# Performance work log

Measured on AMD Instinct MI355X. Metric: run time of the kernel, lower is better.

Reference implementation:

```python
import jax, jax.numpy as jnp
import numpy as np
from jax import lax

K2 = 3                 # support_kernel_size
TARGET_OCC = 0.5
OCC_W = 10.0
ITERS = 10             # flood-fill iterations
THRESH = 0.5
STEEP = 20.0

# 6-neighbor 3D cross kernel (plus-shaped), shape [O=1, I=1, 3, 3, 3]
_cross_np = np.zeros((1, 1, 3, 3, 3), dtype=np.float32)
for dz, dy, dx in [(0, 1, 1), (2, 1, 1), (1, 0, 1), (1, 2, 1), (1, 1, 0), (1, 1, 2)]:
    _cross_np[0, 0, dz, dy, dx] = 1.0


def _conv3d(x, k, pad):
    # x: [B, C, D, H, W], k: [O, I, kd, kh, kw]
    return lax.conv_general_dilated(
        x, k, window_strides=(1, 1, 1), padding=pad,
        dimension_numbers=('NCDHW', 'OIDHW', 'NCDHW'))


def setup_inputs() -> dict:
    key = jax.random.key(0)
    voxel_grid = jax.random.uniform(key, (4, 1, 128, 128, 128), dtype=jnp.float32)
    return {"voxel_grid": voxel_grid}


def reference(voxel_grid):
    B, C, D, H, W = voxel_grid.shape
    N = B * D * H * W
    dt = voxel_grid.dtype

    # ---- overhang score: vectorized over all z-slices at once ----
    # per-slice conv2d(3x3 ones) == conv3d with kernel depth 1
    k2 = jnp.ones((1, 1, 1, K2, K2), dt)
    below = voxel_grid[:, :, :-1]          # [B,1,D-1,H,W]
    curr = voxel_grid[:, :, 1:]
    below_support = _conv3d(below, k2, ((0, 0), (1, 1), (1, 1)))
    support_ratio = below_support / (K2 * K2)
    overhang = (curr * (1.0 - support_ratio)).sum() / N

    # ---- surface area score ----
    k3 = jnp.ones((1, 1, 3, 3, 3), dt)
    neighbor_solid = _conv3d(voxel_grid, k3, ((1, 1), (1, 1), (1, 1)))
    surface_term = neighbor_solid.sum() / 27.0 / N

    occupancy = voxel_grid.sum() / N
    occupancy_penalty = OCC_W * (occupancy - TARGET_OCC) ** 2

    # differentiable flood-fill (diff_find_enclosed_voids)
    seed = jnp.zeros_like(voxel_grid).at[:, :, 5, 5, 5].set(1.0)
    cross = jnp.asarray(_cross_np, dt)
    not_solid = 1.0 - voxel_grid

    def body(i, mask):
        c = _conv3d(mask, cross, ((1, 1), (1, 1), (1, 1)))
        act = jax.nn.sigmoid(STEEP * (c - THRESH))
        return jnp.maximum(mask, act) * not_solid

    enclosed = lax.fori_loop(0, ITERS, body, seed)
    resin_trap_penalty = 100.0 * enclosed.sum() / N

    surface_score = surface_term - resin_trap_penalty - occupancy_penalty
    return overhang, surface_score
```

## Files before the change

### kernel.cpp

```cpp
#include <hip/hip_runtime.h>

#define HW    (128*128)
#define DHW   (128*128*128)
#define NTOT  (4*DHW)
#define NBLK  1024

__device__ __forceinline__ float sigf(float x){ return 1.0f/(1.0f+__expf(-x)); }
__device__ __forceinline__ float4 ld4(const float* p){ return *(const float4*)p; }


__global__ __launch_bounds__(256, 4) void mega_k(
    const float* __restrict__ v, float* __restrict__ p_occ,
    float* __restrict__ p_surf, float* __restrict__ p_over,
    float* __restrict__ p_trap)
{
    __shared__ float4 smem4[1445];
    __shared__ float sred[16];
    float* smem = (float*)smem4;

    const int bid = blockIdx.x;
    const int tid = threadIdx.x;
    const float4 zero4 = make_float4(0,0,0,0);

    if (bid < 4) {
        const int b = bid;
        const size_t gb = (size_t)b * DHW;
        const int ty = tid & 15, tz = tid >> 4;
        const float a_lo = sigf(-10.0f), a_hi = sigf(10.0f);
        #define M(zz,yy) (smem + (((zz)*17 + (yy))*20))

        float m[16], nv[16];
        {
            const float* rv = v + gb + ((size_t)tz*128 + ty)*128;
            int dzy = abs(tz-5) + abs(ty-5);
            #pragma unroll
            for (int q = 0; q < 4; ++q) {
                int x4 = 4*q;
                float4 a = ld4(rv + x4);
                nv[x4+0]=1.f-a.x; nv[x4+1]=1.f-a.y; nv[x4+2]=1.f-a.z; nv[x4+3]=1.f-a.w;
                int d0=dzy+abs(x4+0-5), d1=dzy+abs(x4+1-5);
                int d2=dzy+abs(x4+2-5), d3=dzy+abs(x4+3-5);
                m[x4+0] = ((d0==0)?1.f:((d0==1)?a_hi:a_lo)) * nv[x4+0];
                m[x4+1] = ((d1==0)?1.f:((d1==1)?a_hi:a_lo)) * nv[x4+1];
                m[x4+2] = ((d2==0)?1.f:((d2==1)?a_hi:a_lo)) * nv[x4+2];
                m[x4+3] = ((d3==0)?1.f:((d3==1)?a_hi:a_lo)) * nv[x4+3];
                *(float4*)(M(tz,ty) + x4) = make_float4(m[x4+0],m[x4+1],m[x4+2],m[x4+3]);
            }
        }
        const float xrE = a_lo * (1.f - v[gb + ((size_t)tz*128 + ty)*128 + 16]);
        {
            int a = tid >> 4, e = tid & 15;
            M(16,a)[e] = a_lo * (1.f - v[gb + ((size_t)16*128 + a)*128 + e]);
            M(a,16)[e] = a_lo * (1.f - v[gb + ((size_t)a*128 + 16)*128 + e]);
        }
        __syncthreads();

        for (int it = 0; it < 9; ++it) {
            const float* YM = M(tz,ty-1);
            const float* YP = M(tz,ty+1);
            const float* ZM = M(tz-1,ty);
            const float* ZP = M(tz+1,ty);
            float nm[16];
            #pragma unroll
            for (int q = 0; q < 4; ++q) {
                int x4 = 4*q;
                float4 ym = (ty > 0) ? *(const float4*)(YM + x4) : zero4;
                float4 yp = *(const float4*)(YP + x4);
                float4 zm = (tz > 0) ? *(const float4*)(ZM + x4) : zero4;
                float4 zp = *(const float4*)(ZP + x4);
                float xl = (q == 0) ? 0.f : m[x4-1];
                float xr = (q == 3) ? xrE : m[x4+4];
                float s0 = xl      + m[x4+1] + ym.x + yp.x + zm.x + zp.x;
                float s1 = m[x4+0] + m[x4+2] + ym.y + yp.y + zm.y + zp.y;
                float s2 = m[x4+1] + m[x4+3] + ym.z + yp.z + zm.z + zp.z;
                float s3 = m[x4+2] + xr      + ym.w + yp.w + zm.w + zp.w;
                nm[x4+0] = fmaxf(m[x4+0], sigf(20.f*s0 - 10.f)) * nv[x4+0];
                nm[x4+1] = fmaxf(m[x4+1], sigf(20.f*s1 - 10.f)) * nv[x4+1];
                nm[x4+2] = fmaxf(m[x4+2], sigf(20.f*s2 - 10.f)) * nv[x4+2];
                nm[x4+3] = fmaxf(m[x4+3], sigf(20.f*s3 - 10.f)) * nv[x4+3];
            }
            __syncthreads();
            float* W = M(tz,ty);
            #pragma unroll
            for (int q = 0; q < 4; ++q) {
                int x4 = 4*q;
                *(float4*)(W + x4) = make_float4(nm[x4+0],nm[x4+1],nm[x4+2],nm[x4+3]);
                m[x4+0]=nm[x4+0]; m[x4+1]=nm[x4+1]; m[x4+2]=nm[x4+2]; m[x4+3]=nm[x4+3];
            }
            __syncthreads();
        }

        float d = 0.f;
        #pragma unroll
        for (int x = 0; x < 16; ++x) d += m[x] - a_lo * nv[x];
        #pragma unroll
        for (int o = 32; o; o >>= 1) d += __shfl_down(d, o, 64);
        int lane = tid & 63, wid = tid >> 6;
        if (lane == 0) sred[wid] = d;
        __syncthreads();
        if (tid == 0) p_trap[b] = sred[0] + sred[1] + sred[2] + sred[3];
        #undef M
    } else {
        const int rid = bid - 4;
        const int b   = rid >> 8;
        const int rem = rid & 255;
        const int z0  = (rem >> 4) * 8;
        const int y0  = (rem & 15) * 8;
        const int tx  = tid & 31;
        const int tz  = tid >> 5;
        const int z   = z0 + tz;
        const int x4  = tx * 4;
        const size_t gb = (size_t)b * DHW;
        const float* cp = v + gb + (size_t)z * HW;
        const float* bp = cp - HW;

        float occ = 0.f, surf = 0.f, over = 0.f;

        float4 qb[10];
        if (z >= 1) {
            #pragma unroll
            for (int r = 0; r < 10; ++r) {
                int gy = y0 - 1 + r;
                qb[r] = ((unsigned)gy <= 127u) ? ld4(bp + gy*128 + x4) : zero4;
            }
        }
        float4 qc[8];
        #pragma unroll
        for (int i = 0; i < 8; ++i) qc[i] = ld4(cp + (y0+i)*128 + x4);

        float4 P[10];
        if (z >= 1) {
            #pragma unroll
            for (int r = 0; r < 10; ++r) {
                float4 q = qb[r];
                float ql = __shfl_up(q.w, 1);   if (tx == 0)  ql = 0.f;
                float qr = __shfl_down(q.x, 1); if (tx == 31) qr = 0.f;
                P[r] = make_float4(ql+q.x+q.y, q.x+q.y+q.z,
                                   q.y+q.z+q.w, q.z+q.w+qr);
            }
        }

        const float wz  = (z==0 || z==127) ? 2.f : 3.f;
        const float wx0 = (x4==0)   ? 2.f : 3.f;
        const float wx3 = (x4==124) ? 2.f : 3.f;
        const float inv9 = 1.f/9.f;
        #pragma unroll
        for (int i = 0; i < 8; ++i) {
            const int y = y0 + i;
            float4 val = qc[i];
            occ += val.x + val.y + val.z + val.w;
            float wy = (y==0 || y==127) ? 2.f : 3.f;
            surf += wz*wy*(wx0*val.x + 3.f*val.y + 3.f*val.z + wx3*val.w);
            if (z >= 1) {
                float4 a = P[i], c = P[i+1], d = P[i+2];
                float4 S = make_float4(a.x+c.x+d.x, a.y+c.y+d.y,
                                       a.z+c.z+d.z, a.w+c.w+d.w);
                over += val.x*(1.f - S.x*inv9) + val.y*(1.f - S.y*inv9)
                      + val.z*(1.f - S.z*inv9) + val.w*(1.f - S.w*inv9);
            }
        }

        #pragma unroll
        for (int o = 32; o; o >>= 1) {
            occ  += __shfl_down(occ,  o, 64);
            surf += __shfl_down(surf, o, 64);
            over += __shfl_down(over, o, 64);
        }
        int lane = tid & 63, wid = tid >> 6;
        if (lane == 0) { sred[wid]=occ; sred[4+wid]=surf; sred[8+wid]=over; }
        __syncthreads();
        if (tid == 0) {
            p_occ [rid] = sred[0]+sred[1]+sred[2]+sred[3];
            p_surf[rid] = sred[4]+sred[5]+sred[6]+sred[7];
            p_over[rid] = sred[8]+sred[9]+sred[10]+sred[11];
        }
    }
}

__global__ __launch_bounds__(1024) void finalize_k(
    const float* __restrict__ p_occ, const float* __restrict__ p_surf,
    const float* __restrict__ p_over, const float* __restrict__ p_trap,
    float* __restrict__ out)
{
    double occ=0, surf=0, over=0;
    for (int i = threadIdx.x; i < NBLK; i += 1024) {
        occ += p_occ[i]; surf += p_surf[i]; over += p_over[i];
    }
    __shared__ double sm[3][16];
    #pragma unroll
    for (int o = 32; o; o >>= 1) {
        occ  += __shfl_down(occ,  o, 64);
        surf += __shfl_down(surf, o, 64);
        over += __shfl_down(over, o, 64);
    }
    int lane = threadIdx.x & 63, wid = threadIdx.x >> 6;
    if (lane == 0) { sm[0][wid]=occ; sm[1][wid]=surf; sm[2][wid]=over; }
    __syncthreads();
    if (threadIdx.x == 0) {
        double so=0, ss=0, sv=0;
        for (int w = 0; w < 16; ++w) { so+=sm[0][w]; ss+=sm[1][w]; sv+=sm[2][w]; }
        double dS = (double)p_trap[0] + p_trap[1] + p_trap[2] + p_trap[3];
        double a_lo = 1.0 / (1.0 + exp(10.0));
        double N = (double)NTOT;
        double trap_sum = a_lo * (N - so) + dS;
        double occupancy = so / N;
        double occ_pen = 10.0 * (occupancy - 0.5) * (occupancy - 0.5);
        out[0] = (float)(sv / N);
        out[1] = (float)(ss / 27.0 / N - 100.0 * trap_sum / N - occ_pen);
    }
}

extern "C" void kernel_launch(void* const* d_in, const int* in_sizes, int n_in,
                              void* d_out, int out_size, void* d_ws, size_t ws_size,
                              hipStream_t stream)
{
    const float* v = (const float*)d_in[0];
    float* out = (float*)d_out;
    float* ws = (float*)d_ws;

    float* p_occ  = ws;
    float* p_surf = p_occ  + NBLK;
    float* p_over = p_surf + NBLK;
    float* p_trap = p_over + NBLK;

    mega_k<<<NBLK + 4, 256, 0, stream>>>(v, p_occ, p_surf, p_over, p_trap);
    finalize_k<<<1, 1024, 0, stream>>>(p_occ, p_surf, p_over, p_trap, out);
}
```

Measured before the change: 83.43 us.

## Fuse finalize into main kernel via last-block atomic reduction

Removes the separate finalize kernel launch. Each block atomically adds its partial sums into striped double accumulators in device globals, and the last block to arrive, found through an acq_rel counter, computes the outputs and resets the accumulators. The overhang stencil also switches from precomputing all ten x-summed rows to a rolling three-row window, which lowers register pressure. The cost is global double atomics and relaxed loads in the last block, whose visibility relies on the acquire-release ordering of the counter.

New measurement: 116.9 us. 1.4x slower.

```diff
diff --git a/kernel.cpp b/kernel.cpp
--- a/kernel.cpp
+++ b/kernel.cpp
@@ -4,15 +4,17 @@
 #define DHW   (128*128*128)
 #define NTOT  (4*DHW)
 #define NBLK  1024
+#define TOTB  (NBLK + 4)
+
+__device__ unsigned g_done = 0;
+__device__ double g_acc[3][8];
+__device__ double g_trap;
 
 __device__ __forceinline__ float sigf(float x){ return 1.0f/(1.0f+__expf(-x)); }
 __device__ __forceinline__ float4 ld4(const float* p){ return *(const float4*)p; }
 
-
 __global__ __launch_bounds__(256, 4) void mega_k(
-    const float* __restrict__ v, float* __restrict__ p_occ,
-    float* __restrict__ p_surf, float* __restrict__ p_over,
-    float* __restrict__ p_trap)
+    const float* __restrict__ v, float* __restrict__ out)
 {
     __shared__ float4 smem4[1445];
     __shared__ float sred[16];
@@ -21,6 +23,8 @@
     const int bid = blockIdx.x;
     const int tid = threadIdx.x;
     const float4 zero4 = make_float4(0,0,0,0);
+
+    float occB = 0.f, surfB = 0.f, overB = 0.f, trapB = 0.f;
 
     if (bid < 4) {
         const int b = bid;
@@ -98,7 +102,7 @@
         int lane = tid & 63, wid = tid >> 6;
         if (lane == 0) sred[wid] = d;
         __syncthreads();
-        if (tid == 0) p_trap[b] = sred[0] + sred[1] + sred[2] + sred[3];
+        if (tid == 0) trapB = sred[0] + sred[1] + sred[2] + sred[3];
         #undef M
     } else {
         const int rid = bid - 4;
@@ -128,35 +132,37 @@
         #pragma unroll
         for (int i = 0; i < 8; ++i) qc[i] = ld4(cp + (y0+i)*128 + x4);
 
-        float4 P[10];
-        if (z >= 1) {
-            #pragma unroll
-            for (int r = 0; r < 10; ++r) {
-                float4 q = qb[r];
-                float ql = __shfl_up(q.w, 1);   if (tx == 0)  ql = 0.f;
-                float qr = __shfl_down(q.x, 1); if (tx == 31) qr = 0.f;
-                P[r] = make_float4(ql+q.x+q.y, q.x+q.y+q.z,
-                                   q.y+q.z+q.w, q.z+q.w+qr);
-            }
-        }
+        auto xsum = [&](float4 q) -> float4 {
+            float ql = __shfl_up(q.w, 1);   if (tx == 0)  ql = 0.f;
+            float qr = __shfl_down(q.x, 1); if (tx == 31) qr = 0.f;
+            return make_float4(ql+q.x+q.y, q.x+q.y+q.z, q.y+q.z+q.w, q.z+q.w+qr);
+        };
 
         const float wz  = (z==0 || z==127) ? 2.f : 3.f;
         const float wx0 = (x4==0)   ? 2.f : 3.f;
         const float wx3 = (x4==124) ? 2.f : 3.f;
         const float inv9 = 1.f/9.f;
+
         #pragma unroll
         for (int i = 0; i < 8; ++i) {
-            const int y = y0 + i;
             float4 val = qc[i];
             occ += val.x + val.y + val.z + val.w;
-            float wy = (y==0 || y==127) ? 2.f : 3.f;
+            float wy = ((y0+i)==0 || (y0+i)==127) ? 2.f : 3.f;
             surf += wz*wy*(wx0*val.x + 3.f*val.y + 3.f*val.z + wx3*val.w);
-            if (z >= 1) {
-                float4 a = P[i], c = P[i+1], d = P[i+2];
-                float4 S = make_float4(a.x+c.x+d.x, a.y+c.y+d.y,
-                                       a.z+c.z+d.z, a.w+c.w+d.w);
+        }
+
+        if (z >= 1) {
+            float4 P0 = xsum(qb[0]);
+            float4 P1 = xsum(qb[1]);
+            #pragma unroll
+            for (int i = 0; i < 8; ++i) {
+                float4 P2 = xsum(qb[i+2]);
+                float4 val = qc[i];
+                float4 S = make_float4(P0.x+P1.x+P2.x, P0.y+P1.y+P2.y,
+                                       P0.z+P1.z+P2.z, P0.w+P1.w+P2.w);
                 over += val.x*(1.f - S.x*inv9) + val.y*(1.f - S.y*inv9)
                       + val.z*(1.f - S.z*inv9) + val.w*(1.f - S.w*inv9);
+                P0 = P1; P1 = P2;
             }
         }
 
@@ -170,43 +176,46 @@
         if (lane == 0) { sred[wid]=occ; sred[4+wid]=surf; sred[8+wid]=over; }
         __syncthreads();
         if (tid == 0) {
-            p_occ [rid] = sred[0]+sred[1]+sred[2]+sred[3];
-            p_surf[rid] = sred[4]+sred[5]+sred[6]+sred[7];
-            p_over[rid] = sred[8]+sred[9]+sred[10]+sred[11];
+            occB  = sred[0]+sred[1]+sred[2]+sred[3];
+            surfB = sred[4]+sred[5]+sred[6]+sred[7];
+            overB = sred[8]+sred[9]+sred[10]+sred[11];
         }
     }
-}
-
-__global__ __launch_bounds__(1024) void finalize_k(
-    const float* __restrict__ p_occ, const float* __restrict__ p_surf,
-    const float* __restrict__ p_over, const float* __restrict__ p_trap,
-    float* __restrict__ out)
-{
-    double occ=0, surf=0, over=0;
-    for (int i = threadIdx.x; i < NBLK; i += 1024) {
-        occ += p_occ[i]; surf += p_surf[i]; over += p_over[i];
-    }
-    __shared__ double sm[3][16];
-    #pragma unroll
-    for (int o = 32; o; o >>= 1) {
-        occ  += __shfl_down(occ,  o, 64);
-        surf += __shfl_down(surf, o, 64);
-        over += __shfl_down(over, o, 64);
-    }
-    int lane = threadIdx.x & 63, wid = threadIdx.x >> 6;
-    if (lane == 0) { sm[0][wid]=occ; sm[1][wid]=surf; sm[2][wid]=over; }
-    __syncthreads();
-    if (threadIdx.x == 0) {
-        double so=0, ss=0, sv=0;
-        for (int w = 0; w < 16; ++w) { so+=sm[0][w]; ss+=sm[1][w]; sv+=sm[2][w]; }
-        double dS = (double)p_trap[0] + p_trap[1] + p_trap[2] + p_trap[3];
-        double a_lo = 1.0 / (1.0 + exp(10.0));
-        double N = (double)NTOT;
-        double trap_sum = a_lo * (N - so) + dS;
-        double occupancy = so / N;
-        double occ_pen = 10.0 * (occupancy - 0.5) * (occupancy - 0.5);
-        out[0] = (float)(sv / N);
-        out[1] = (float)(ss / 27.0 / N - 100.0 * trap_sum / N - occ_pen);
+
+    if (tid == 0) {
+        if (bid < 4) {
+            atomicAdd(&g_trap, (double)trapB);
+        } else {
+            int s = bid & 7;
+            atomicAdd(&g_acc[0][s], (double)occB);
+            atomicAdd(&g_acc[1][s], (double)surfB);
+            atomicAdd(&g_acc[2][s], (double)overB);
+        }
+        unsigned old = __hip_atomic_fetch_add(&g_done, 1u, __ATOMIC_ACQ_REL,
+                                              __HIP_MEMORY_SCOPE_AGENT);
+        if ((old + 1u) % (unsigned)TOTB == 0u) {
+            double so = 0, ss = 0, sv = 0;
+            for (int i = 0; i < 8; ++i) {
+                so += __hip_atomic_load(&g_acc[0][i], __ATOMIC_RELAXED, __HIP_MEMORY_SCOPE_AGENT);
+                ss += __hip_atomic_load(&g_acc[1][i], __ATOMIC_RELAXED, __HIP_MEMORY_SCOPE_AGENT);
+                sv += __hip_atomic_load(&g_acc[2][i], __ATOMIC_RELAXED, __HIP_MEMORY_SCOPE_AGENT);
+            }
+            double dS = __hip_atomic_load(&g_trap, __ATOMIC_RELAXED, __HIP_MEMORY_SCOPE_AGENT);
+            for (int i = 0; i < 8; ++i) {
+                __hip_atomic_store(&g_acc[0][i], 0.0, __ATOMIC_RELAXED, __HIP_MEMORY_SCOPE_AGENT);
+                __hip_atomic_store(&g_acc[1][i], 0.0, __ATOMIC_RELAXED, __HIP_MEMORY_SCOPE_AGENT);
+                __hip_atomic_store(&g_acc[2][i], 0.0, __ATOMIC_RELAXED, __HIP_MEMORY_SCOPE_AGENT);
+            }
+            __hip_atomic_store(&g_trap, 0.0, __ATOMIC_RELAXED, __HIP_MEMORY_SCOPE_AGENT);
+
+            double a_lo = 1.0 / (1.0 + exp(10.0));
+            double N = (double)NTOT;
+            double trap_sum = a_lo * (N - so) + dS;
+            double occupancy = so / N;
+            double occ_pen = 10.0 * (occupancy - 0.5) * (occupancy - 0.5);
+            out[0] = (float)(sv / N);
+            out[1] = (float)(ss / 27.0 / N - 100.0 * trap_sum / N - occ_pen);
+        }
     }
 }
 
@@ -216,13 +225,7 @@
 {
     const float* v = (const float*)d_in[0];
     float* out = (float*)d_out;
-    float* ws = (float*)d_ws;
-
-    float* p_occ  = ws;
-    float* p_surf = p_occ  + NBLK;
-    float* p_over = p_surf + NBLK;
-    float* p_trap = p_over + NBLK;
-
-    mega_k<<<NBLK + 4, 256, 0, stream>>>(v, p_occ, p_surf, p_over, p_trap);
-    finalize_k<<<1, 1024, 0, stream>>>(p_occ, p_surf, p_over, p_trap, out);
+    (void)d_ws; (void)ws_size;
+
+    mega_k<<<TOTB, 256, 0, stream>>>(v, out);
 }
```
